# Kernel optimization log

Measured on AMD Instinct MI355X. Metric: run time of the kernel, lower is better.

Reference implementation:

```python
import jax, jax.numpy as jnp
import numpy as np

N_NODES = 100000

def gin_conv(x, edge_index, W, b):
    # PyG GINConv with eps=0: out = Linear(x + sum_{j->i} x_j)
    src, dst = edge_index[0], edge_index[1]
    agg = jax.ops.segment_sum(x[src], dst, num_segments=N_NODES)  # [N, d]
    return (x + agg) @ W + b

def setup_inputs() -> dict:
    key = jax.random.key(0)
    ks = jax.random.split(key, 8)
    x = jax.random.normal(ks[0], (N_NODES, 32), dtype=jnp.float32)
    edge_index = jax.random.randint(ks[1], (2, 1600000), 0, N_NODES, dtype=jnp.int64)
    def lin(k, fan_in, fan_out):
        kw, kb = jax.random.split(k)
        lim = 1.0 / np.sqrt(fan_in)
        W = jax.random.uniform(kw, (fan_in, fan_out), minval=-lim, maxval=lim, dtype=jnp.float32)
        b = jax.random.uniform(kb, (fan_out,), minval=-lim, maxval=lim, dtype=jnp.float32)
        return W, b
    W1, b1 = lin(ks[2], 32, 64)
    W2, b2 = lin(ks[3], 64, 64)
    W3, b3 = lin(ks[4], 64, 10)
    return {"x": x, "edge_index": edge_index,
            "W1": W1, "b1": b1, "W2": W2, "b2": b2, "W3": W3, "b3": b3}

def reference(x, edge_index, W1, b1, W2, b2, W3, b3):
    h = jax.nn.relu(gin_conv(x, edge_index, W1, b1))
    h = jax.nn.relu(gin_conv(h, edge_index, W2, b2))
    return gin_conv(h, edge_index, W3, b3)  # [N, classes] logits
```

## Files before the change

kernel.cpp:

```cpp
#include <hip/hip_runtime.h>


#define GIN_N 100000
#define NBUCKET 256
#define NB2 391
#define BSTRIDE 8192
#define EPT 16

typedef unsigned short bfu;
typedef float v2f __attribute__((ext_vector_type(2)));

__device__ __forceinline__ float bf_lo(unsigned int u) {
    return __uint_as_float(u << 16);
}
__device__ __forceinline__ float bf_hi(unsigned int u) {
    return __uint_as_float(u & 0xffff0000u);
}
__device__ __forceinline__ unsigned int f2bf(float f) {
    unsigned int u = __float_as_uint(f);
    return (u + 0x7fffu + ((u >> 16) & 1u)) >> 16;
}
__device__ __forceinline__ v2f fp8lo(unsigned u) {
    return __builtin_amdgcn_cvt_pk_f32_fp8(u, false);
}
__device__ __forceinline__ v2f fp8hi(unsigned u) {
    return __builtin_amdgcn_cvt_pk_f32_fp8(u, true);
}

template <int S>
__device__ __forceinline__ void blelloch_excl(int* a) {
#pragma unroll
    for (int d = 1; d < S; d <<= 1) {
        __syncthreads();
        int idx = (threadIdx.x + 1) * (d << 1) - 1;
        if (idx < S) a[idx] += a[idx - d];
    }
    __syncthreads();
    if (threadIdx.x == 0) a[S - 1] = 0;
#pragma unroll
    for (int d = S >> 1; d >= 1; d >>= 1) {
        __syncthreads();
        int idx = (threadIdx.x + 1) * (d << 1) - 1;
        if (idx < S) {
            int t = a[idx - d];
            a[idx - d] = a[idx];
            a[idx] += t;
        }
    }
    __syncthreads();
}

__global__ void f2q_kernel(const float* __restrict__ in,
                           unsigned* __restrict__ outq, int n8,
                           int* __restrict__ cursor) {
    int t = blockIdx.x * blockDim.x + threadIdx.x;
    if (blockIdx.x == 0) cursor[threadIdx.x] = 0;
    if (t >= n8) return;
    const float4* v = reinterpret_cast<const float4*>(in);
    float4 a = v[2 * t], b = v[2 * t + 1];
    unsigned w0 = 0, w1 = 0;
    w0 = __builtin_amdgcn_cvt_pk_fp8_f32(a.x, a.y, w0, false);
    w0 = __builtin_amdgcn_cvt_pk_fp8_f32(a.z, a.w, w0, true);
    w1 = __builtin_amdgcn_cvt_pk_fp8_f32(b.x, b.y, w1, false);
    w1 = __builtin_amdgcn_cvt_pk_fp8_f32(b.z, b.w, w1, true);
    reinterpret_cast<uint2*>(outq)[t] = make_uint2(w0, w1);
}

__global__ __launch_bounds__(256) void bucket_kernel(
        const int* __restrict__ src, const int* __restrict__ dst, int E,
        unsigned* __restrict__ bucketbuf, int* __restrict__ cursor) {
    __shared__ int h[NBUCKET];
    __shared__ int base[NBUCKET];
    int tid = threadIdx.x;
    int chunk0 = blockIdx.x * (256 * EPT);
    h[tid] = 0;
    __syncthreads();
    int myb[EPT];
    unsigned myrec[EPT];
#pragma unroll
    for (int i = 0; i < EPT; ++i) {
        int e = chunk0 + tid + i * 256;
        if (e < E) {
            int d = dst[e];
            int s = src[e];
            int b = d / NB2;
            myb[i] = b;
            myrec[i] = ((unsigned)(d - b * NB2) << 17) | (unsigned)s;
            atomicAdd(&h[b], 1);
        } else {
            myb[i] = -1;
        }
    }
    __syncthreads();
    base[tid] = atomicAdd(&cursor[tid], h[tid]);
    h[tid] = 0;
    __syncthreads();
#pragma unroll
    for (int i = 0; i < EPT; ++i) {
        int b = myb[i];
        if (b < 0) continue;
        int pos = base[b] + atomicAdd(&h[b], 1);
        if (pos < BSTRIDE) bucketbuf[(size_t)b * BSTRIDE + pos] = myrec[i];
    }
}

__global__ __launch_bounds__(256) void csr_build_kernel(
        const unsigned* __restrict__ bucketbuf,
        const int* __restrict__ cursor,
        int* __restrict__ rowptr,
        int* __restrict__ adj) {
    __shared__ int csr[BSTRIDE];
    __shared__ int cnt[512];
    __shared__ int off[512];
    __shared__ int bscan[NBUCKET];
    int b = blockIdx.x;
    int tid = threadIdx.x;
    bscan[tid] = cursor[tid];
    int mycnt = cursor[b];
    if (mycnt > BSTRIDE) mycnt = BSTRIDE;
    blelloch_excl<NBUCKET>(bscan);
    int base = bscan[b];

    const unsigned* buf = bucketbuf + (size_t)b * BSTRIDE;
    cnt[tid] = 0;
    cnt[tid + 256] = 0;
    __syncthreads();
    for (int i = tid; i < mycnt; i += 256)
        atomicAdd(&cnt[buf[i] >> 17], 1);
    __syncthreads();
    off[tid] = cnt[tid];
    off[tid + 256] = cnt[tid + 256];
    blelloch_excl<512>(off);

    int nodes0 = b * NB2;
    int nn2 = GIN_N + 1 - nodes0;
    if (nn2 > NB2) nn2 = NB2;
    for (int l = tid; l < nn2; l += 256) rowptr[nodes0 + l] = base + off[l];
    __syncthreads();

    for (int i = tid; i < mycnt; i += 256) {
        unsigned r = buf[i];
        int pos = atomicAdd(&off[r >> 17], 1);
        csr[pos] = (int)(r & 0x1FFFFu);
    }
    __syncthreads();
    for (int i = tid; i < mycnt; i += 256) adj[base + i] = csr[i];
}

__global__ __launch_bounds__(256, 8) void fused1_kernel(
        const float* __restrict__ xf,
        const unsigned* __restrict__ xq,
        const int* __restrict__ rowptr,
        const int* __restrict__ adj,
        const float* __restrict__ W,
        const float* __restrict__ b,
        bfu* __restrict__ outb,
        unsigned* __restrict__ outq) {
    constexpr int K = 32, M = 64;
    constexpr int TPN = 4, NODES = 64, TP2 = 4, MT = 16;
    constexpr int STR = K + 4;

    __shared__ unsigned Wp[K * M / 2];
    __shared__ float bs[M];
    __shared__ float tile[NODES * STR];

    for (int i = threadIdx.x; i < K * M / 2; i += 256) {
        float w0 = W[2 * i], w1 = W[2 * i + 1];
        Wp[i] = f2bf(w0) | (f2bf(w1) << 16);
    }
    if (threadIdx.x < M) bs[threadIdx.x] = b[threadIdx.x];

    int node0 = blockIdx.x * NODES;
    int tid = threadIdx.x;

    {
        int l = tid / TPN;
        int j = tid % TPN;
        int n = node0 + l;
        if (n < GIN_N) {
            int start = rowptr[n];
            int d = rowptr[n + 1] - start;
            const int* row = adj + start;
            const uint2* fq = reinterpret_cast<const uint2*>(xq);
            v2f a0, a1, a2, a3;
            {
                const float4* xv = reinterpret_cast<const float4*>(xf);
                float4 a = xv[(size_t)n * 8 + 2 * j];
                float4 c = xv[(size_t)n * 8 + 2 * j + 1];
                a0 = v2f{a.x, a.y}; a1 = v2f{a.z, a.w};
                a2 = v2f{c.x, c.y}; a3 = v2f{c.z, c.w};
            }
            int k = 0;
            for (; k + 4 <= d; k += 4) {
                uint2 v0 = fq[(size_t)row[k] * 4 + j];
                uint2 v1 = fq[(size_t)row[k + 1] * 4 + j];
                uint2 v2 = fq[(size_t)row[k + 2] * 4 + j];
                uint2 v3 = fq[(size_t)row[k + 3] * 4 + j];
                a0 += fp8lo(v0.x) + fp8lo(v1.x) + fp8lo(v2.x) + fp8lo(v3.x);
                a1 += fp8hi(v0.x) + fp8hi(v1.x) + fp8hi(v2.x) + fp8hi(v3.x);
                a2 += fp8lo(v0.y) + fp8lo(v1.y) + fp8lo(v2.y) + fp8lo(v3.y);
                a3 += fp8hi(v0.y) + fp8hi(v1.y) + fp8hi(v2.y) + fp8hi(v3.y);
            }
            for (; k < d; ++k) {
                uint2 v = fq[(size_t)row[k] * 4 + j];
                a0 += fp8lo(v.x); a1 += fp8hi(v.x);
                a2 += fp8lo(v.y); a3 += fp8hi(v.y);
            }
            float* tp = &tile[l * STR + j * 8];
            tp[0] = a0.x; tp[1] = a0.y; tp[2] = a1.x; tp[3] = a1.y;
            tp[4] = a2.x; tp[5] = a2.y; tp[6] = a3.x; tp[7] = a3.y;
        }
    }
    __syncthreads();

    {
        int l = tid / TP2;
        int sub = tid % TP2;
        int n = node0 + l;
        if (n >= GIN_N) return;
        float acc[MT];
#pragma unroll
        for (int jj = 0; jj < MT; ++jj) acc[jj] = bs[sub * MT + jj];
        const float* tp = &tile[l * STR];
#pragma unroll
        for (int k = 0; k < K; ++k) {
            float v = tp[k];
            const unsigned* wr = &Wp[k * (M / 2) + sub * (MT / 2)];
#pragma unroll
            for (int j2 = 0; j2 < MT / 2; ++j2) {
                unsigned wp = wr[j2];
                acc[2 * j2]     = fmaf(v, bf_lo(wp), acc[2 * j2]);
                acc[2 * j2 + 1] = fmaf(v, bf_hi(wp), acc[2 * j2 + 1]);
            }
        }
#pragma unroll
        for (int jj = 0; jj < MT; ++jj) acc[jj] = fmaxf(acc[jj], 0.0f);
        unsigned pb[MT / 2];
#pragma unroll
        for (int j2 = 0; j2 < MT / 2; ++j2)
            pb[j2] = f2bf(acc[2 * j2]) | (f2bf(acc[2 * j2 + 1]) << 16);
        uint4* ob = reinterpret_cast<uint4*>(outb + (size_t)n * 64 + sub * MT);
        ob[0] = make_uint4(pb[0], pb[1], pb[2], pb[3]);
        ob[1] = make_uint4(pb[4], pb[5], pb[6], pb[7]);
        unsigned q[4];
#pragma unroll
        for (int q4 = 0; q4 < 4; ++q4) {
            unsigned w = 0;
            w = __builtin_amdgcn_cvt_pk_fp8_f32(acc[4 * q4], acc[4 * q4 + 1], w, false);
            w = __builtin_amdgcn_cvt_pk_fp8_f32(acc[4 * q4 + 2], acc[4 * q4 + 3], w, true);
            q[q4] = w;
        }
        reinterpret_cast<uint4*>(outq)[(size_t)n * 4 + sub] =
            make_uint4(q[0], q[1], q[2], q[3]);
    }
}

__global__ __launch_bounds__(256, 8) void fused2_kernel(
        const bfu* __restrict__ xb,
        const unsigned* __restrict__ xq,
        const int* __restrict__ rowptr,
        const int* __restrict__ adj,
        const float* __restrict__ W,
        const float* __restrict__ b,
        bfu* __restrict__ out) {
    constexpr int K = 64, M = 64;
    constexpr int TPN = 8, NODES = 32, TP2 = 8, MT = 8;
    constexpr int STR = K + 4;

    __shared__ unsigned Wp[K * M / 2];
    __shared__ float bs[M];
    __shared__ float tile[NODES * STR];

    for (int i = threadIdx.x; i < K * M / 2; i += 256) {
        float w0 = W[2 * i], w1 = W[2 * i + 1];
        Wp[i] = f2bf(w0) | (f2bf(w1) << 16);
    }
    if (threadIdx.x < M) bs[threadIdx.x] = b[threadIdx.x];

    int node0 = blockIdx.x * NODES;
    int tid = threadIdx.x;

    {
        int l = tid / TPN;
        int j = tid % TPN;
        int n = node0 + l;
        if (n < GIN_N) {
            int start = rowptr[n];
            int d = rowptr[n + 1] - start;
            const int* row = adj + start;
            const uint2* fq = reinterpret_cast<const uint2*>(xq);
            v2f a0, a1, a2, a3;
            {
                uint4 u = reinterpret_cast<const uint4*>(xb)[(size_t)n * 8 + j];
                a0 = v2f{bf_lo(u.x), bf_hi(u.x)};
                a1 = v2f{bf_lo(u.y), bf_hi(u.y)};
                a2 = v2f{bf_lo(u.z), bf_hi(u.z)};
                a3 = v2f{bf_lo(u.w), bf_hi(u.w)};
            }
            int k = 0;
            for (; k + 4 <= d; k += 4) {
                uint2 v0 = fq[(size_t)row[k] * 8 + j];
                uint2 v1 = fq[(size_t)row[k + 1] * 8 + j];
                uint2 v2 = fq[(size_t)row[k + 2] * 8 + j];
                uint2 v3 = fq[(size_t)row[k + 3] * 8 + j];
                a0 += fp8lo(v0.x) + fp8lo(v1.x) + fp8lo(v2.x) + fp8lo(v3.x);
                a1 += fp8hi(v0.x) + fp8hi(v1.x) + fp8hi(v2.x) + fp8hi(v3.x);
                a2 += fp8lo(v0.y) + fp8lo(v1.y) + fp8lo(v2.y) + fp8lo(v3.y);
                a3 += fp8hi(v0.y) + fp8hi(v1.y) + fp8hi(v2.y) + fp8hi(v3.y);
            }
            for (; k < d; ++k) {
                uint2 v = fq[(size_t)row[k] * 8 + j];
                a0 += fp8lo(v.x); a1 += fp8hi(v.x);
                a2 += fp8lo(v.y); a3 += fp8hi(v.y);
            }
            float* tp = &tile[l * STR + j * 8];
            tp[0] = a0.x; tp[1] = a0.y; tp[2] = a1.x; tp[3] = a1.y;
            tp[4] = a2.x; tp[5] = a2.y; tp[6] = a3.x; tp[7] = a3.y;
        }
    }
    __syncthreads();

    {
        int l = tid / TP2;
        int sub = tid % TP2;
        int n = node0 + l;
        if (n >= GIN_N) return;
        float acc[MT];
#pragma unroll
        for (int jj = 0; jj < MT; ++jj) acc[jj] = bs[sub * MT + jj];
        const float* tp = &tile[l * STR];
#pragma unroll
        for (int k = 0; k < K; ++k) {
            float v = tp[k];
            const unsigned* wr = &Wp[k * (M / 2) + sub * (MT / 2)];
#pragma unroll
            for (int j2 = 0; j2 < MT / 2; ++j2) {
                unsigned wp = wr[j2];
                acc[2 * j2]     = fmaf(v, bf_lo(wp), acc[2 * j2]);
                acc[2 * j2 + 1] = fmaf(v, bf_hi(wp), acc[2 * j2 + 1]);
            }
        }
        bfu* o = out + (size_t)n * M + sub * MT;
#pragma unroll
        for (int jj = 0; jj < MT; jj += 2) {
            float r0 = fmaxf(acc[jj], 0.0f);
            float r1 = fmaxf(acc[jj + 1], 0.0f);
            unsigned p = f2bf(r0) | (f2bf(r1) << 16);
            *reinterpret_cast<unsigned*>(o + jj) = p;
        }
    }
}

__global__ __launch_bounds__(256) void mlp3_kernel(
        const bfu* __restrict__ xb,
        const float* __restrict__ W,
        bfu* __restrict__ t16) {
    constexpr int K = 64, M = 10, TPN = 2, MT = 5;
    __shared__ float Ws[K * M];
    for (int i = threadIdx.x; i < K * M; i += 256) Ws[i] = W[i];
    __syncthreads();
    int t = blockIdx.x * blockDim.x + threadIdx.x;
    int n = t / TPN;
    int sub = t % TPN;
    if (n >= GIN_N) return;
    float acc[MT] = {0, 0, 0, 0, 0};
#pragma unroll
    for (int kc = 0; kc < K / 8; ++kc) {
        uint4 u = reinterpret_cast<const uint4*>(xb)[(size_t)n * (K / 8) + kc];
        float v[8] = {bf_lo(u.x), bf_hi(u.x), bf_lo(u.y), bf_hi(u.y),
                      bf_lo(u.z), bf_hi(u.z), bf_lo(u.w), bf_hi(u.w)};
#pragma unroll
        for (int kk = 0; kk < 8; ++kk) {
            const float* wr = &Ws[(kc * 8 + kk) * M + sub * MT];
#pragma unroll
            for (int jj = 0; jj < MT; ++jj)
                acc[jj] = fmaf(v[kk], wr[jj], acc[jj]);
        }
    }
    bfu* o = t16 + (size_t)n * 16 + sub * MT;
#pragma unroll
    for (int jj = 0; jj < MT; ++jj) o[jj] = (bfu)f2bf(acc[jj]);
}

__global__ void gather_final_kernel(const unsigned* __restrict__ t8,
                                    const int* __restrict__ rowptr,
                                    const int* __restrict__ adj,
                                    const float* __restrict__ b3,
                                    float* __restrict__ out) {
    int t = blockIdx.x * blockDim.x + threadIdx.x;
    int n = t >> 3;
    int j = t & 7;
    if (n >= GIN_N || j >= 5) return;
    int start = rowptr[n];
    int d = rowptr[n + 1] - start;
    const int* row = adj + start;
    unsigned sv = t8[(size_t)n * 8 + j];
    float a0 = bf_lo(sv), a1 = bf_hi(sv);
    int k = 0;
    for (; k + 4 <= d; k += 4) {
        int r0 = row[k], r1 = row[k + 1], r2 = row[k + 2], r3 = row[k + 3];
        unsigned v0 = t8[(size_t)r0 * 8 + j];
        unsigned v1 = t8[(size_t)r1 * 8 + j];
        unsigned v2 = t8[(size_t)r2 * 8 + j];
        unsigned v3 = t8[(size_t)r3 * 8 + j];
        a0 += bf_lo(v0) + bf_lo(v1) + bf_lo(v2) + bf_lo(v3);
        a1 += bf_hi(v0) + bf_hi(v1) + bf_hi(v2) + bf_hi(v3);
    }
    for (; k < d; ++k) {
        unsigned v = t8[(size_t)row[k] * 8 + j];
        a0 += bf_lo(v); a1 += bf_hi(v);
    }
    out[(size_t)n * 10 + 2 * j] = a0 + b3[2 * j];
    out[(size_t)n * 10 + 2 * j + 1] = a1 + b3[2 * j + 1];
}

extern "C" void kernel_launch(void* const* d_in, const int* in_sizes, int n_in,
                              void* d_out, int out_size, void* d_ws, size_t ws_size,
                              hipStream_t stream) {
    const float* x  = (const float*)d_in[0];
    const int*   ei = (const int*)d_in[1];
    const float* W1 = (const float*)d_in[2];
    const float* b1 = (const float*)d_in[3];
    const float* W2 = (const float*)d_in[4];
    const float* b2 = (const float*)d_in[5];
    const float* W3 = (const float*)d_in[6];
    const float* b3 = (const float*)d_in[7];
    float* out = (float*)d_out;

    const int N = GIN_N;
    const int E = in_sizes[1] / 2;
    const int* src = ei;
    const int* dst = ei + E;

    bfu* H1b = (bfu*)d_ws;
    bfu* H2 = H1b + (size_t)N * 64;
    unsigned* H1q = (unsigned*)(H2 + (size_t)N * 64);
    unsigned* Xq = H1q + (size_t)N * 16;
    bfu* Tb = (bfu*)(Xq + (size_t)N * 8);
    int* rowptr = (int*)(Tb + (size_t)N * 16);
    int* cursor = rowptr + (N + 8);
    int* adj = cursor + 256;
    unsigned* bucketbuf = (unsigned*)(adj + (size_t)E);

    const int BLK = 256;

    f2q_kernel<<<(N * 32 / 8 + BLK - 1) / BLK, BLK, 0, stream>>>(
        x, Xq, N * 32 / 8, cursor);
    {
        int chunk = BLK * EPT;
        bucket_kernel<<<(E + chunk - 1) / chunk, BLK, 0, stream>>>(
            src, dst, E, bucketbuf, cursor);
        csr_build_kernel<<<NBUCKET, BLK, 0, stream>>>(
            bucketbuf, cursor, rowptr, adj);
    }

    fused1_kernel<<<(N + 63) / 64, BLK, 0, stream>>>(
        x, Xq, rowptr, adj, W1, b1, H1b, H1q);

    fused2_kernel<<<(N + 31) / 32, BLK, 0, stream>>>(
        H1b, H1q, rowptr, adj, W2, b2, H2);

    mlp3_kernel<<<(N * 2 + BLK - 1) / BLK, BLK, 0, stream>>>(H2, W3, Tb);
    gather_final_kernel<<<(N * 8 + BLK - 1) / BLK, BLK, 0, stream>>>(
        (const unsigned*)Tb, rowptr, adj, b3, out);
}
```

Measured before the change: 212.7 us.

## Fuse layer-3 linear into layer-2, widen gathers to 16-byte loads, merge preprocessing kernels

Folds the fp32-to-fp8 quantization of x into the edge-bucketing kernel and replaces the cursor reset with a memset. Fuses the W3 projection into the layer-2 kernel using a cross-lane shuffle reduction, which removes the mlp3 kernel and the bf16 H2 round trip. The self term in layer 2 now comes from the fp8 copy, so the bf16 H1 buffer is dropped. The gathers in all three aggregation kernels load 16 bytes per thread per neighbour with 8-way unrolling and use fewer threads per node. This cuts kernel launches and memory traffic and raises memory-level parallelism, but costs more registers and lower occupancy, and the fp8 self term slightly reduces accuracy.

```diff
diff --git a/kernel.cpp b/kernel.cpp
--- a/kernel.cpp
+++ b/kernel.cpp
@@ -25,6 +25,12 @@
 }
 __device__ __forceinline__ v2f fp8hi(unsigned u) {
     return __builtin_amdgcn_cvt_pk_f32_fp8(u, true);
+}
+__device__ __forceinline__ void acc_fp8x16(v2f* a, uint4 v) {
+    a[0] += fp8lo(v.x); a[1] += fp8hi(v.x);
+    a[2] += fp8lo(v.y); a[3] += fp8hi(v.y);
+    a[4] += fp8lo(v.z); a[5] += fp8hi(v.z);
+    a[6] += fp8lo(v.w); a[7] += fp8hi(v.w);
 }
 
 template <int S>
@@ -50,28 +56,27 @@
     __syncthreads();
 }
 
-__global__ void f2q_kernel(const float* __restrict__ in,
-                           unsigned* __restrict__ outq, int n8,
-                           int* __restrict__ cursor) {
-    int t = blockIdx.x * blockDim.x + threadIdx.x;
-    if (blockIdx.x == 0) cursor[threadIdx.x] = 0;
-    if (t >= n8) return;
-    const float4* v = reinterpret_cast<const float4*>(in);
-    float4 a = v[2 * t], b = v[2 * t + 1];
-    unsigned w0 = 0, w1 = 0;
-    w0 = __builtin_amdgcn_cvt_pk_fp8_f32(a.x, a.y, w0, false);
-    w0 = __builtin_amdgcn_cvt_pk_fp8_f32(a.z, a.w, w0, true);
-    w1 = __builtin_amdgcn_cvt_pk_fp8_f32(b.x, b.y, w1, false);
-    w1 = __builtin_amdgcn_cvt_pk_fp8_f32(b.z, b.w, w1, true);
-    reinterpret_cast<uint2*>(outq)[t] = make_uint2(w0, w1);
-}
-
-__global__ __launch_bounds__(256) void bucket_kernel(
+__global__ __launch_bounds__(256) void build_kernel(
         const int* __restrict__ src, const int* __restrict__ dst, int E,
-        unsigned* __restrict__ bucketbuf, int* __restrict__ cursor) {
+        unsigned* __restrict__ bucketbuf, int* __restrict__ cursor,
+        const float* __restrict__ x, unsigned* __restrict__ xq, int n8,
+        int bblk) {
     __shared__ int h[NBUCKET];
     __shared__ int base[NBUCKET];
     int tid = threadIdx.x;
+    if (blockIdx.x >= bblk) {
+        int t = (blockIdx.x - bblk) * 256 + tid;
+        if (t >= n8) return;
+        const float4* v = reinterpret_cast<const float4*>(x);
+        float4 a = v[2 * t], b = v[2 * t + 1];
+        unsigned w0 = 0, w1 = 0;
+        w0 = __builtin_amdgcn_cvt_pk_fp8_f32(a.x, a.y, w0, false);
+        w0 = __builtin_amdgcn_cvt_pk_fp8_f32(a.z, a.w, w0, true);
+        w1 = __builtin_amdgcn_cvt_pk_fp8_f32(b.x, b.y, w1, false);
+        w1 = __builtin_amdgcn_cvt_pk_fp8_f32(b.z, b.w, w1, true);
+        reinterpret_cast<uint2*>(xq)[t] = make_uint2(w0, w1);
+        return;
+    }
     int chunk0 = blockIdx.x * (256 * EPT);
     h[tid] = 0;
     __syncthreads();
@@ -147,17 +152,16 @@
     for (int i = tid; i < mycnt; i += 256) adj[base + i] = csr[i];
 }
 
-__global__ __launch_bounds__(256, 8) void fused1_kernel(
+__global__ __launch_bounds__(256, 7) void fused1_kernel(
         const float* __restrict__ xf,
         const unsigned* __restrict__ xq,
         const int* __restrict__ rowptr,
         const int* __restrict__ adj,
         const float* __restrict__ W,
         const float* __restrict__ b,
-        bfu* __restrict__ outb,
         unsigned* __restrict__ outq) {
     constexpr int K = 32, M = 64;
-    constexpr int TPN = 4, NODES = 64, TP2 = 4, MT = 16;
+    constexpr int NODES = 128, TP2 = 2, MT = 32;
     constexpr int STR = K + 4;
 
     __shared__ unsigned Wp[K * M / 2];
@@ -174,48 +178,61 @@
     int tid = threadIdx.x;
 
     {
-        int l = tid / TPN;
-        int j = tid % TPN;
+        int l = tid >> 1;
+        int j = tid & 1;
         int n = node0 + l;
         if (n < GIN_N) {
             int start = rowptr[n];
             int d = rowptr[n + 1] - start;
             const int* row = adj + start;
-            const uint2* fq = reinterpret_cast<const uint2*>(xq);
-            v2f a0, a1, a2, a3;
+            const uint4* fq = reinterpret_cast<const uint4*>(xq);
+            v2f a[8];
             {
                 const float4* xv = reinterpret_cast<const float4*>(xf);
-                float4 a = xv[(size_t)n * 8 + 2 * j];
-                float4 c = xv[(size_t)n * 8 + 2 * j + 1];
-                a0 = v2f{a.x, a.y}; a1 = v2f{a.z, a.w};
-                a2 = v2f{c.x, c.y}; a3 = v2f{c.z, c.w};
+#pragma unroll
+                for (int c = 0; c < 4; ++c) {
+                    float4 s = xv[(size_t)n * 8 + j * 4 + c];
+                    a[2 * c] = v2f{s.x, s.y};
+                    a[2 * c + 1] = v2f{s.z, s.w};
+                }
             }
             int k = 0;
+            for (; k + 8 <= d; k += 8) {
+                uint4 v0 = fq[(size_t)row[k] * 2 + j];
+                uint4 v1 = fq[(size_t)row[k + 1] * 2 + j];
+                uint4 v2 = fq[(size_t)row[k + 2] * 2 + j];
+                uint4 v3 = fq[(size_t)row[k + 3] * 2 + j];
+                uint4 v4 = fq[(size_t)row[k + 4] * 2 + j];
+                uint4 v5 = fq[(size_t)row[k + 5] * 2 + j];
+                uint4 v6 = fq[(size_t)row[k + 6] * 2 + j];
+                uint4 v7 = fq[(size_t)row[k + 7] * 2 + j];
+                acc_fp8x16(a, v0); acc_fp8x16(a, v1);
+                acc_fp8x16(a, v2); acc_fp8x16(a, v3);
+                acc_fp8x16(a, v4); acc_fp8x16(a, v5);
+                acc_fp8x16(a, v6); acc_fp8x16(a, v7);
+            }
             for (; k + 4 <= d; k += 4) {
-                uint2 v0 = fq[(size_t)row[k] * 4 + j];
-                uint2 v1 = fq[(size_t)row[k + 1] * 4 + j];
-                uint2 v2 = fq[(size_t)row[k + 2] * 4 + j];
-                uint2 v3 = fq[(size_t)row[k + 3] * 4 + j];
-                a0 += fp8lo(v0.x) + fp8lo(v1.x) + fp8lo(v2.x) + fp8lo(v3.x);
-                a1 += fp8hi(v0.x) + fp8hi(v1.x) + fp8hi(v2.x) + fp8hi(v3.x);
-                a2 += fp8lo(v0.y) + fp8lo(v1.y) + fp8lo(v2.y) + fp8lo(v3.y);
-                a3 += fp8hi(v0.y) + fp8hi(v1.y) + fp8hi(v2.y) + fp8hi(v3.y);
-            }
-            for (; k < d; ++k) {
-                uint2 v = fq[(size_t)row[k] * 4 + j];
-                a0 += fp8lo(v.x); a1 += fp8hi(v.x);
-                a2 += fp8lo(v.y); a3 += fp8hi(v.y);
-            }
-            float* tp = &tile[l * STR + j * 8];
-            tp[0] = a0.x; tp[1] = a0.y; tp[2] = a1.x; tp[3] = a1.y;
-            tp[4] = a2.x; tp[5] = a2.y; tp[6] = a3.x; tp[7] = a3.y;
+                uint4 v0 = fq[(size_t)row[k] * 2 + j];
+                uint4 v1 = fq[(size_t)row[k + 1] * 2 + j];
+                uint4 v2 = fq[(size_t)row[k + 2] * 2 + j];
+                uint4 v3 = fq[(size_t)row[k + 3] * 2 + j];
+                acc_fp8x16(a, v0); acc_fp8x16(a, v1);
+                acc_fp8x16(a, v2); acc_fp8x16(a, v3);
+            }
+            for (; k < d; ++k) acc_fp8x16(a, fq[(size_t)row[k] * 2 + j]);
+            float* tp = &tile[l * STR + j * 16];
+#pragma unroll
+            for (int q = 0; q < 8; ++q) {
+                tp[2 * q] = a[q].x;
+                tp[2 * q + 1] = a[q].y;
+            }
         }
     }
     __syncthreads();
 
     {
-        int l = tid / TP2;
-        int sub = tid % TP2;
+        int l = tid >> 1;
+        int sub = tid & 1;
         int n = node0 + l;
         if (n >= GIN_N) return;
         float acc[MT];
@@ -235,94 +252,100 @@
         }
 #pragma unroll
         for (int jj = 0; jj < MT; ++jj) acc[jj] = fmaxf(acc[jj], 0.0f);
-        unsigned pb[MT / 2];
-#pragma unroll
-        for (int j2 = 0; j2 < MT / 2; ++j2)
-            pb[j2] = f2bf(acc[2 * j2]) | (f2bf(acc[2 * j2 + 1]) << 16);
-        uint4* ob = reinterpret_cast<uint4*>(outb + (size_t)n * 64 + sub * MT);
-        ob[0] = make_uint4(pb[0], pb[1], pb[2], pb[3]);
-        ob[1] = make_uint4(pb[4], pb[5], pb[6], pb[7]);
-        unsigned q[4];
-#pragma unroll
-        for (int q4 = 0; q4 < 4; ++q4) {
+        unsigned q[8];
+#pragma unroll
+        for (int q4 = 0; q4 < 8; ++q4) {
             unsigned w = 0;
             w = __builtin_amdgcn_cvt_pk_fp8_f32(acc[4 * q4], acc[4 * q4 + 1], w, false);
             w = __builtin_amdgcn_cvt_pk_fp8_f32(acc[4 * q4 + 2], acc[4 * q4 + 3], w, true);
             q[q4] = w;
         }
-        reinterpret_cast<uint4*>(outq)[(size_t)n * 4 + sub] =
-            make_uint4(q[0], q[1], q[2], q[3]);
-    }
-}
-
-__global__ __launch_bounds__(256, 8) void fused2_kernel(
-        const bfu* __restrict__ xb,
+        uint4* oq = reinterpret_cast<uint4*>(outq) + (size_t)n * 4 + sub * 2;
+        oq[0] = make_uint4(q[0], q[1], q[2], q[3]);
+        oq[1] = make_uint4(q[4], q[5], q[6], q[7]);
+    }
+}
+
+__global__ __launch_bounds__(256, 5) void fused2t_kernel(
         const unsigned* __restrict__ xq,
         const int* __restrict__ rowptr,
         const int* __restrict__ adj,
         const float* __restrict__ W,
         const float* __restrict__ b,
-        bfu* __restrict__ out) {
+        const float* __restrict__ W3,
+        unsigned* __restrict__ tout) {
     constexpr int K = 64, M = 64;
-    constexpr int TPN = 8, NODES = 32, TP2 = 8, MT = 8;
+    constexpr int NODES = 64, TP2 = 4, MT = 16;
     constexpr int STR = K + 4;
 
     __shared__ unsigned Wp[K * M / 2];
     __shared__ float bs[M];
+    __shared__ float W3s[K * 10];
     __shared__ float tile[NODES * STR];
 
     for (int i = threadIdx.x; i < K * M / 2; i += 256) {
         float w0 = W[2 * i], w1 = W[2 * i + 1];
         Wp[i] = f2bf(w0) | (f2bf(w1) << 16);
     }
+    for (int i = threadIdx.x; i < K * 10; i += 256) W3s[i] = W3[i];
     if (threadIdx.x < M) bs[threadIdx.x] = b[threadIdx.x];
 
     int node0 = blockIdx.x * NODES;
     int tid = threadIdx.x;
 
     {
-        int l = tid / TPN;
-        int j = tid % TPN;
+        int l = tid >> 2;
+        int j = tid & 3;
         int n = node0 + l;
         if (n < GIN_N) {
             int start = rowptr[n];
             int d = rowptr[n + 1] - start;
             const int* row = adj + start;
-            const uint2* fq = reinterpret_cast<const uint2*>(xq);
-            v2f a0, a1, a2, a3;
+            const uint4* fq = reinterpret_cast<const uint4*>(xq);
+            v2f a[8];
             {
-                uint4 u = reinterpret_cast<const uint4*>(xb)[(size_t)n * 8 + j];
-                a0 = v2f{bf_lo(u.x), bf_hi(u.x)};
-                a1 = v2f{bf_lo(u.y), bf_hi(u.y)};
-                a2 = v2f{bf_lo(u.z), bf_hi(u.z)};
-                a3 = v2f{bf_lo(u.w), bf_hi(u.w)};
+                uint4 s = fq[(size_t)n * 4 + j];
+#pragma unroll
+                for (int q = 0; q < 8; ++q) a[q] = v2f{0.f, 0.f};
+                acc_fp8x16(a, s);
             }
             int k = 0;
+            for (; k + 8 <= d; k += 8) {
+                uint4 v0 = fq[(size_t)row[k] * 4 + j];
+                uint4 v1 = fq[(size_t)row[k + 1] * 4 + j];
+                uint4 v2 = fq[(size_t)row[k + 2] * 4 + j];
+                uint4 v3 = fq[(size_t)row[k + 3] * 4 + j];
+                uint4 v4 = fq[(size_t)row[k + 4] * 4 + j];
+                uint4 v5 = fq[(size_t)row[k + 5] * 4 + j];
+                uint4 v6 = fq[(size_t)row[k + 6] * 4 + j];
+                uint4 v7 = fq[(size_t)row[k + 7] * 4 + j];
+                acc_fp8x16(a, v0); acc_fp8x16(a, v1);
+                acc_fp8x16(a, v2); acc_fp8x16(a, v3);
+                acc_fp8x16(a, v4); acc_fp8x16(a, v5);
+                acc_fp8x16(a, v6); acc_fp8x16(a, v7);
+            }
             for (; k + 4 <= d; k += 4) {
-                uint2 v0 = fq[(size_t)row[k] * 8 + j];
-                uint2 v1 = fq[(size_t)row[k + 1] * 8 + j];
-                uint2 v2 = fq[(size_t)row[k + 2] * 8 + j];
-                uint2 v3 = fq[(size_t)row[k + 3] * 8 + j];
-                a0 += fp8lo(v0.x) + fp8lo(v1.x) + fp8lo(v2.x) + fp8lo(v3.x);
-                a1 += fp8hi(v0.x) + fp8hi(v1.x) + fp8hi(v2.x) + fp8hi(v3.x);
-                a2 += fp8lo(v0.y) + fp8lo(v1.y) + fp8lo(v2.y) + fp8lo(v3.y);
-                a3 += fp8hi(v0.y) + fp8hi(v1.y) + fp8hi(v2.y) + fp8hi(v3.y);
-            }
-            for (; k < d; ++k) {
-                uint2 v = fq[(size_t)row[k] * 8 + j];
-                a0 += fp8lo(v.x); a1 += fp8hi(v.x);
-                a2 += fp8lo(v.y); a3 += fp8hi(v.y);
-            }
-            float* tp = &tile[l * STR + j * 8];
-            tp[0] = a0.x; tp[1] = a0.y; tp[2] = a1.x; tp[3] = a1.y;
-            tp[4] = a2.x; tp[5] = a2.y; tp[6] = a3.x; tp[7] = a3.y;
+                uint4 v0 = fq[(size_t)row[k] * 4 + j];
+                uint4 v1 = fq[(size_t)row[k + 1] * 4 + j];
+                uint4 v2 = fq[(size_t)row[k + 2] * 4 + j];
+                uint4 v3 = fq[(size_t)row[k + 3] * 4 + j];
+                acc_fp8x16(a, v0); acc_fp8x16(a, v1);
+                acc_fp8x16(a, v2); acc_fp8x16(a, v3);
+            }
+            for (; k < d; ++k) acc_fp8x16(a, fq[(size_t)row[k] * 4 + j]);
+            float* tp = &tile[l * STR + j * 16];
+#pragma unroll
+            for (int q = 0; q < 8; ++q) {
+                tp[2 * q] = a[q].x;
+                tp[2 * q + 1] = a[q].y;
+            }
         }
     }
     __syncthreads();
 
     {
-        int l = tid / TP2;
-        int sub = tid % TP2;
+        int l = tid >> 2;
+        int sub = tid & 3;
         int n = node0 + l;
         if (n >= GIN_N) return;
         float acc[MT];
@@ -340,78 +363,96 @@
                 acc[2 * j2 + 1] = fmaf(v, bf_hi(wp), acc[2 * j2 + 1]);
             }
         }
-        bfu* o = out + (size_t)n * M + sub * MT;
-#pragma unroll
-        for (int jj = 0; jj < MT; jj += 2) {
-            float r0 = fmaxf(acc[jj], 0.0f);
-            float r1 = fmaxf(acc[jj + 1], 0.0f);
-            unsigned p = f2bf(r0) | (f2bf(r1) << 16);
-            *reinterpret_cast<unsigned*>(o + jj) = p;
-        }
-    }
-}
-
-__global__ __launch_bounds__(256) void mlp3_kernel(
-        const bfu* __restrict__ xb,
-        const float* __restrict__ W,
-        bfu* __restrict__ t16) {
-    constexpr int K = 64, M = 10, TPN = 2, MT = 5;
-    __shared__ float Ws[K * M];
-    for (int i = threadIdx.x; i < K * M; i += 256) Ws[i] = W[i];
-    __syncthreads();
+#pragma unroll
+        for (int jj = 0; jj < MT; ++jj) acc[jj] = fmaxf(acc[jj], 0.0f);
+        float pt[10];
+#pragma unroll
+        for (int jj = 0; jj < 10; ++jj) pt[jj] = 0.0f;
+#pragma unroll
+        for (int kk = 0; kk < MT; ++kk) {
+            float v = acc[kk];
+            const float* wr = &W3s[(sub * MT + kk) * 10];
+#pragma unroll
+            for (int jj = 0; jj < 10; ++jj) pt[jj] = fmaf(v, wr[jj], pt[jj]);
+        }
+#pragma unroll
+        for (int jj = 0; jj < 10; ++jj) {
+            float v = pt[jj];
+            v += __shfl_xor(v, 1, 64);
+            v += __shfl_xor(v, 2, 64);
+            pt[jj] = v;
+        }
+        if (sub == 0) {
+            unsigned p[8];
+#pragma unroll
+            for (int j2 = 0; j2 < 5; ++j2)
+                p[j2] = f2bf(pt[2 * j2]) | (f2bf(pt[2 * j2 + 1]) << 16);
+            p[5] = 0; p[6] = 0; p[7] = 0;
+            uint4* o = reinterpret_cast<uint4*>(tout) + (size_t)n * 2;
+            o[0] = make_uint4(p[0], p[1], p[2], p[3]);
+            o[1] = make_uint4(p[4], p[5], p[6], p[7]);
+        }
+    }
+}
+
+__global__ __launch_bounds__(256, 8) void gather_final_kernel(
+        const unsigned* __restrict__ t8,
+        const int* __restrict__ rowptr,
+        const int* __restrict__ adj,
+        const float* __restrict__ b3,
+        float* __restrict__ out) {
     int t = blockIdx.x * blockDim.x + threadIdx.x;
-    int n = t / TPN;
-    int sub = t % TPN;
+    int n = t >> 1;
+    int j = t & 1;
     if (n >= GIN_N) return;
-    float acc[MT] = {0, 0, 0, 0, 0};
-#pragma unroll
-    for (int kc = 0; kc < K / 8; ++kc) {
-        uint4 u = reinterpret_cast<const uint4*>(xb)[(size_t)n * (K / 8) + kc];
-        float v[8] = {bf_lo(u.x), bf_hi(u.x), bf_lo(u.y), bf_hi(u.y),
-                      bf_lo(u.z), bf_hi(u.z), bf_lo(u.w), bf_hi(u.w)};
-#pragma unroll
-        for (int kk = 0; kk < 8; ++kk) {
-            const float* wr = &Ws[(kc * 8 + kk) * M + sub * MT];
-#pragma unroll
-            for (int jj = 0; jj < MT; ++jj)
-                acc[jj] = fmaf(v[kk], wr[jj], acc[jj]);
-        }
-    }
-    bfu* o = t16 + (size_t)n * 16 + sub * MT;
-#pragma unroll
-    for (int jj = 0; jj < MT; ++jj) o[jj] = (bfu)f2bf(acc[jj]);
-}
-
-__global__ void gather_final_kernel(const unsigned* __restrict__ t8,
-                                    const int* __restrict__ rowptr,
-                                    const int* __restrict__ adj,
-                                    const float* __restrict__ b3,
-                                    float* __restrict__ out) {
-    int t = blockIdx.x * blockDim.x + threadIdx.x;
-    int n = t >> 3;
-    int j = t & 7;
-    if (n >= GIN_N || j >= 5) return;
     int start = rowptr[n];
     int d = rowptr[n + 1] - start;
     const int* row = adj + start;
-    unsigned sv = t8[(size_t)n * 8 + j];
-    float a0 = bf_lo(sv), a1 = bf_hi(sv);
+    const uint4* T = reinterpret_cast<const uint4*>(t8);
+    v2f a[4];
+    {
+        uint4 s = T[(size_t)n * 2 + j];
+        a[0] = v2f{bf_lo(s.x), bf_hi(s.x)};
+        a[1] = v2f{bf_lo(s.y), bf_hi(s.y)};
+        a[2] = v2f{bf_lo(s.z), bf_hi(s.z)};
+        a[3] = v2f{bf_lo(s.w), bf_hi(s.w)};
+    }
     int k = 0;
-    for (; k + 4 <= d; k += 4) {
-        int r0 = row[k], r1 = row[k + 1], r2 = row[k + 2], r3 = row[k + 3];
-        unsigned v0 = t8[(size_t)r0 * 8 + j];
-        unsigned v1 = t8[(size_t)r1 * 8 + j];
-        unsigned v2 = t8[(size_t)r2 * 8 + j];
-        unsigned v3 = t8[(size_t)r3 * 8 + j];
-        a0 += bf_lo(v0) + bf_lo(v1) + bf_lo(v2) + bf_lo(v3);
-        a1 += bf_hi(v0) + bf_hi(v1) + bf_hi(v2) + bf_hi(v3);
+    for (; k + 8 <= d; k += 8) {
+        uint4 v0 = T[(size_t)row[k] * 2 + j];
+        uint4 v1 = T[(size_t)row[k + 1] * 2 + j];
+        uint4 v2 = T[(size_t)row[k + 2] * 2 + j];
+        uint4 v3 = T[(size_t)row[k + 3] * 2 + j];
+        uint4 v4 = T[(size_t)row[k + 4] * 2 + j];
+        uint4 v5 = T[(size_t)row[k + 5] * 2 + j];
+        uint4 v6 = T[(size_t)row[k + 6] * 2 + j];
+        uint4 v7 = T[(size_t)row[k + 7] * 2 + j];
+#define ACC_T(v) \
+        a[0] += v2f{bf_lo(v.x), bf_hi(v.x)}; \
+        a[1] += v2f{bf_lo(v.y), bf_hi(v.y)}; \
+        a[2] += v2f{bf_lo(v.z), bf_hi(v.z)}; \
+        a[3] += v2f{bf_lo(v.w), bf_hi(v.w)};
+        ACC_T(v0) ACC_T(v1) ACC_T(v2) ACC_T(v3)
+        ACC_T(v4) ACC_T(v5) ACC_T(v6) ACC_T(v7)
     }
     for (; k < d; ++k) {
-        unsigned v = t8[(size_t)row[k] * 8 + j];
-        a0 += bf_lo(v); a1 += bf_hi(v);
-    }
-    out[(size_t)n * 10 + 2 * j] = a0 + b3[2 * j];
-    out[(size_t)n * 10 + 2 * j + 1] = a1 + b3[2 * j + 1];
+        uint4 v = T[(size_t)row[k] * 2 + j];
+        ACC_T(v)
+    }
+#undef ACC_T
+    float* o = out + (size_t)n * 10 + j * 8;
+    if (j == 0) {
+        const float2* b2v = reinterpret_cast<const float2*>(b3);
+#pragma unroll
+        for (int c = 0; c < 4; ++c) {
+            float2 bb = b2v[c];
+            reinterpret_cast<float2*>(o)[c] =
+                make_float2(a[c].x + bb.x, a[c].y + bb.y);
+        }
+    } else {
+        reinterpret_cast<float2*>(o)[0] =
+            make_float2(a[0].x + b3[8], a[0].y + b3[9]);
+    }
 }
 
 extern "C" void kernel_launch(void* const* d_in, const int* in_sizes, int n_in,
@@ -432,35 +473,33 @@
     const int* src = ei;
     const int* dst = ei + E;
 
-    bfu* H1b = (bfu*)d_ws;
-    bfu* H2 = H1b + (size_t)N * 64;
-    unsigned* H1q = (unsigned*)(H2 + (size_t)N * 64);
-    unsigned* Xq = H1q + (size_t)N * 16;
-    bfu* Tb = (bfu*)(Xq + (size_t)N * 8);
-    int* rowptr = (int*)(Tb + (size_t)N * 16);
+    unsigned* Xq = (unsigned*)d_ws;
+    unsigned* H1q = Xq + (size_t)N * 8;
+    unsigned* Tb = H1q + (size_t)N * 16;
+    int* rowptr = (int*)(Tb + (size_t)N * 8);
     int* cursor = rowptr + (N + 8);
     int* adj = cursor + 256;
     unsigned* bucketbuf = (unsigned*)(adj + (size_t)E);
 
     const int BLK = 256;
 
-    f2q_kernel<<<(N * 32 / 8 + BLK - 1) / BLK, BLK, 0, stream>>>(
-        x, Xq, N * 32 / 8, cursor);
+    hipMemsetAsync(cursor, 0, 256 * sizeof(int), stream);
     {
-        int chunk = BLK * EPT;
-        bucket_kernel<<<(E + chunk - 1) / chunk, BLK, 0, stream>>>(
-            src, dst, E, bucketbuf, cursor);
+        int n8 = N * 32 / 8;
+        int bblk = (E + BLK * EPT - 1) / (BLK * EPT);
+        int xblk = (n8 + BLK - 1) / BLK;
+        build_kernel<<<bblk + xblk, BLK, 0, stream>>>(
+            src, dst, E, bucketbuf, cursor, x, Xq, n8, bblk);
         csr_build_kernel<<<NBUCKET, BLK, 0, stream>>>(
             bucketbuf, cursor, rowptr, adj);
     }
 
-    fused1_kernel<<<(N + 63) / 64, BLK, 0, stream>>>(
-        x, Xq, rowptr, adj, W1, b1, H1b, H1q);
-
-    fused2_kernel<<<(N + 31) / 32, BLK, 0, stream>>>(
-        H1b, H1q, rowptr, adj, W2, b2, H2);
-
-    mlp3_kernel<<<(N * 2 + BLK - 1) / BLK, BLK, 0, stream>>>(H2, W3, Tb);
-    gather_final_kernel<<<(N * 8 + BLK - 1) / BLK, BLK, 0, stream>>>(
-        (const unsigned*)Tb, rowptr, adj, b3, out);
-}
+    fused1_kernel<<<(N + 127) / 128, BLK, 0, stream>>>(
+        x, Xq, rowptr, adj, W1, b1, H1q);
+
+    fused2t_kernel<<<(N + 63) / 64, BLK, 0, stream>>>(
+        H1q, rowptr, adj, W2, b2, W3, Tb);
+
+    gather_final_kernel<<<(N * 2 + BLK - 1) / BLK, BLK, 0, stream>>>(
+        Tb, rowptr, adj, b3, out);
+}
```

After: 323.4 us. 1.52x slower.
